# Kernel tuning notes

Hardware: AMD Instinct MI355X
Metric: run time of the kernel (lower is better)

The kernel has to match this reference:

```python
import jax, jax.numpy as jnp
import numpy as np

N_NODES = 50000
N_EDGES = 1600000
IN_DIM, HID_DIM, OUT_DIM = 512, 128, 16


def spmm(edge_src, edge_dst, edge_vals, x):
    # sparse.mm(A, x): out[dst] += A[dst, src] * x[src]
    msgs = edge_vals[:, None] * x[edge_src]  # [E, D]
    return jax.ops.segment_sum(msgs, edge_dst, num_segments=N_NODES)


def setup_inputs() -> dict:
    key = jax.random.key(0)
    k1, k2, k3, k4, k5, k6 = jax.random.split(key, 6)
    feature = jax.random.normal(k1, (N_NODES, IN_DIM), dtype=jnp.float32)
    edge_src = jax.random.randint(k2, (N_EDGES,), 0, N_NODES, dtype=jnp.int32)
    edge_dst = jax.random.randint(k3, (N_EDGES,), 0, N_NODES, dtype=jnp.int32)
    edge_vals = jax.random.uniform(k4, (N_EDGES,), dtype=jnp.float32)
    # kaiming_uniform-style init: bound = sqrt(6 / fan_in) (a=sqrt(5) omitted for simplicity of scale)
    b1 = float(np.sqrt(6.0 / IN_DIM))
    b2 = float(np.sqrt(6.0 / HID_DIM))
    W1 = jax.random.uniform(k5, (IN_DIM, HID_DIM), dtype=jnp.float32, minval=-b1, maxval=b1)
    W2 = jax.random.uniform(k6, (HID_DIM, OUT_DIM), dtype=jnp.float32, minval=-b2, maxval=b2)
    return {"feature": feature, "edge_src": edge_src, "edge_dst": edge_dst,
            "edge_vals": edge_vals, "W1": W1, "W2": W2}


def reference(feature, edge_src, edge_dst, edge_vals, W1, W2):
    # layer 1: dense matmul -> sparse aggregation -> ReLU
    h = jax.nn.relu(spmm(edge_src, edge_dst, edge_vals, feature @ W1))
    # layer 2
    out = spmm(edge_src, edge_dst, edge_vals, h @ W2)
    return out
```

## Files before the change

kernel.cpp:

```cpp
#include <hip/hip_runtime.h>

#define N_NODES 50000
#define N_EDGES 1600000
#define IN_DIM 512
#define HID_DIM 128
#define OUT_DIM 16

#define BKT_SHIFT 6
#define BKT_NODES 64
#define NB ((N_NODES + BKT_NODES - 1) / BKT_NODES)
#define SC_EDGES 8192
#define SC_BLOCKS ((N_EDGES + SC_EDGES - 1) / SC_EDGES)
#define PREP_BLOCKS ((IN_DIM * HID_DIM + 1023) / 1024)
#define NS_CAP 2560
#define MG_GEMM_BLOCKS ((N_NODES + 127) / 128)

typedef __attribute__((ext_vector_type(8))) __bf16 bf16x8;
typedef __attribute__((ext_vector_type(4))) __bf16 bf16x4;
typedef __attribute__((ext_vector_type(8))) unsigned short ushort8;
typedef __attribute__((ext_vector_type(4))) float f32x4;
typedef __attribute__((ext_vector_type(2))) float f32x2;

static __device__ __forceinline__ unsigned short f2bf(float x) {
    unsigned int u = __float_as_uint(x);
    u += 0x7FFFu + ((u >> 16) & 1u);
    return (unsigned short)(u >> 16);
}
static __device__ __forceinline__ float bf2f(unsigned short v) {
    return __uint_as_float(((unsigned int)v) << 16);
}
static __device__ __forceinline__ unsigned char f2fp8(float x) {
    int pk = __builtin_amdgcn_cvt_pk_fp8_f32(x, x, 0, false);
    return (unsigned char)(pk & 0xFF);
}

__device__ inline int wave_incl_scan(int v) {
    #pragma unroll
    for (int off = 1; off < 64; off <<= 1) {
        int x = __shfl_up(v, off, 64);
        if ((threadIdx.x & 63) >= off) v += x;
    }
    return v;
}


__global__ void zero_bcnt_kernel(int* __restrict__ bcnt) {
    int t = threadIdx.x;
    if (t < NB) bcnt[t] = 0;
}

__global__ __launch_bounds__(1024) void hist_prep_kernel(const int* __restrict__ dst,
                                                         int* __restrict__ bcnt,
                                                         int* __restrict__ blk_hist_T,
                                                         const float* __restrict__ W1,
                                                         unsigned short* __restrict__ Wt) {
    if (blockIdx.x >= SC_BLOCKS) {
        int i = (blockIdx.x - SC_BLOCKS) * 1024 + threadIdx.x;
        if (i < IN_DIM * HID_DIM) {
            int k = i >> 7, col = i & 127;
            Wt[(size_t)col * IN_DIM + k] = f2bf(W1[i]);
        }
        return;
    }
    __shared__ int lc[NB];
    const int t = threadIdx.x;
    for (int b = t; b < NB; b += 1024) lc[b] = 0;
    __syncthreads();
    const int eb = blockIdx.x * SC_EDGES + t * 8;
    #pragma unroll
    for (int q = 0; q < 2; q++) {
        int e0 = eb + q * 4;
        if (e0 + 4 <= N_EDGES) {
            int4 d4 = *(const int4*)&dst[e0];
            atomicAdd(&lc[d4.x >> BKT_SHIFT], 1);
            atomicAdd(&lc[d4.y >> BKT_SHIFT], 1);
            atomicAdd(&lc[d4.z >> BKT_SHIFT], 1);
            atomicAdd(&lc[d4.w >> BKT_SHIFT], 1);
        } else {
            for (int k = 0; k < 4; k++) {
                int e = e0 + k;
                if (e < N_EDGES) atomicAdd(&lc[dst[e] >> BKT_SHIFT], 1);
            }
        }
    }
    __syncthreads();
    for (int b = t; b < NB; b += 1024) {
        int c = lc[b];
        blk_hist_T[(size_t)b * SC_BLOCKS + blockIdx.x] = c;
        if (c) atomicAdd(&bcnt[b], c);
    }
}

__global__ __launch_bounds__(1024) void bucket_scan_kernel(const int* __restrict__ bcnt,
                                                           int* __restrict__ bucket_ptr) {
    __shared__ int wsums[16];
    const int t = threadIdx.x;
    const int lane = t & 63, wid = t >> 6;
    int v = (t < NB) ? bcnt[t] : 0;
    int incl = wave_incl_scan(v);
    if (lane == 63) wsums[wid] = incl;
    __syncthreads();
    if (wid == 0) {
        int wv = (lane < 16) ? wsums[lane] : 0;
        int ws = wave_incl_scan(wv);
        if (lane < 16) wsums[lane] = ws;
    }
    __syncthreads();
    int woff = wid ? wsums[wid - 1] : 0;
    int excl = woff + incl - v;
    if (t < NB) bucket_ptr[t] = excl;
    if (t == NB - 1) bucket_ptr[NB] = excl + v;
}

__global__ __launch_bounds__(512) void base_scan_kernel(const int* __restrict__ bucket_ptr,
                                                        int* __restrict__ blk_hist_T) {
    const int lane = threadIdx.x & 63;
    const int b = blockIdx.x * 8 + (threadIdx.x >> 6);
    if (b >= NB) return;
    int* row = blk_hist_T + (size_t)b * SC_BLOCKS;
    int carry = bucket_ptr[b];
    for (int c0 = 0; c0 < SC_BLOCKS; c0 += 64) {
        int idx = c0 + lane;
        int v = (idx < SC_BLOCKS) ? row[idx] : 0;
        int incl = wave_incl_scan(v);
        if (idx < SC_BLOCKS) row[idx] = carry + incl - v;
        carry += __shfl(incl, 63, 64);
    }
}


#define G1_XSTR 72
#define G1_BSTR 72
__global__ __launch_bounds__(512) void scatter_gemm1_kernel(const float* __restrict__ X,
                                                            const unsigned short* __restrict__ Wt,
                                                            unsigned char* __restrict__ h0,
                                                            const int* __restrict__ src,
                                                            const int* __restrict__ dst,
                                                            const float* __restrict__ val,
                                                            const int* __restrict__ blk_hist_T,
                                                            int2* __restrict__ pairs_bkt) {
    if (blockIdx.x < MG_GEMM_BLOCKS) {
        __shared__ __align__(16) unsigned short Xs[128 * G1_XSTR];
        __shared__ __align__(16) unsigned short Bs[128 * G1_BSTR];
        const int t = threadIdx.x;
        const int lane = t & 63;
        const int wave = t >> 6;
        const int wr = wave >> 2;
        const int wc = wave & 3;
        const int c = lane & 15, g = lane >> 4;
        const int m0 = blockIdx.x * 128;

        f32x4 acc[4][2];
        #pragma unroll
        for (int mt = 0; mt < 4; mt++)
            #pragma unroll
            for (int nt = 0; nt < 2; nt++) acc[mt][nt] = (f32x4){0.f, 0.f, 0.f, 0.f};

        float4 xrA[4], xrB[4];
        ushort8 brA[2], brB[2];

        #define G1_LOAD(XR, BR, kt)                                                          \
            _Pragma("unroll")                                                                \
            for (int p = 0; p < 4; p++) {                                                    \
                int idx = p * 512 + t;                                                       \
                int xrow = idx >> 4, xseg = idx & 15;                                        \
                int grow = m0 + xrow; grow = (grow < N_NODES) ? grow : (N_NODES - 1);        \
                XR[p] = *(const float4*)&X[(size_t)grow * IN_DIM + (kt) * 64 + xseg * 4];    \
            }                                                                                \
            _Pragma("unroll")                                                                \
            for (int p = 0; p < 2; p++) {                                                    \
                int idx = p * 512 + t;                                                       \
                int bcol = idx >> 3, bseg = idx & 7;                                         \
                BR[p] = *(const ushort8*)&Wt[(size_t)bcol * IN_DIM + (kt) * 64 + bseg * 8];  \
            }

        #define G1_WRITE(XR, BR)                                                             \
            _Pragma("unroll")                                                                \
            for (int p = 0; p < 4; p++) {                                                    \
                int idx = p * 512 + t;                                                       \
                int xrow = idx >> 4, xseg = idx & 15;                                        \
                bf16x4 xw;                                                                   \
                xw[0] = (__bf16)XR[p].x; xw[1] = (__bf16)XR[p].y;                            \
                xw[2] = (__bf16)XR[p].z; xw[3] = (__bf16)XR[p].w;                            \
                *(bf16x4*)&Xs[xrow * G1_XSTR + xseg * 4] = xw;                               \
            }                                                                                \
            _Pragma("unroll")                                                                \
            for (int p = 0; p < 2; p++) {                                                    \
                int idx = p * 512 + t;                                                       \
                int bcol = idx >> 3, bseg = idx & 7;                                         \
                *(ushort8*)&Bs[bcol * G1_BSTR + bseg * 8] = BR[p];                           \
            }

        G1_LOAD(xrA, brA, 0)
        G1_LOAD(xrB, brB, 1)
        #pragma unroll
        for (int kt = 0; kt < 8; kt++) {
            if (kt & 1) { G1_WRITE(xrB, brB) } else { G1_WRITE(xrA, brA) }
            __syncthreads();
            if (kt + 2 < 8) {
                if (kt & 1) { G1_LOAD(xrB, brB, kt + 2) } else { G1_LOAD(xrA, brA, kt + 2) }
            }
            #pragma unroll
            for (int ks = 0; ks < 2; ks++) {
                bf16x8 bf[2];
                #pragma unroll
                for (int nt = 0; nt < 2; nt++) {
                    int col = wc * 32 + nt * 16 + c;
                    bf[nt] = *(const bf16x8*)&Bs[col * G1_BSTR + ks * 32 + g * 8];
                }
                #pragma unroll
                for (int mt = 0; mt < 4; mt++) {
                    bf16x8 af = *(const bf16x8*)&Xs[(wr * 64 + mt * 16 + c) * G1_XSTR + ks * 32 + g * 8];
                    #pragma unroll
                    for (int nt = 0; nt < 2; nt++)
                        acc[mt][nt] = __builtin_amdgcn_mfma_f32_16x16x32_bf16(af, bf[nt],
                                                                              acc[mt][nt], 0, 0, 0);
                }
            }
            __syncthreads();
        }
        #undef G1_LOAD
        #undef G1_WRITE

        #pragma unroll
        for (int mt = 0; mt < 4; mt++) {
            #pragma unroll
            for (int r = 0; r < 4; r++) {
                int row = m0 + wr * 64 + mt * 16 + g * 4 + r;
                if (row < N_NODES) {
                    #pragma unroll
                    for (int nt = 0; nt < 2; nt++) {
                        int col = wc * 32 + nt * 16 + c;
                        h0[(size_t)row * HID_DIM + col] = f2fp8(acc[mt][nt][r]);
                    }
                }
            }
        }
    } else {
        __shared__ int cbase[NB];
        const int sb = blockIdx.x - MG_GEMM_BLOCKS;
        const int t = threadIdx.x;
        for (int b = t; b < NB; b += 512)
            cbase[b] = blk_hist_T[(size_t)b * SC_BLOCKS + sb];
        __syncthreads();
        const int eb = sb * SC_EDGES + t * 16;
        #pragma unroll
        for (int q = 0; q < 4; q++) {
            int e0 = eb + q * 4;
            if (e0 + 4 <= N_EDGES) {
                int4 s4 = *(const int4*)&src[e0];
                int4 d4 = *(const int4*)&dst[e0];
                float4 v4 = *(const float4*)&val[e0];
                #pragma unroll
                for (int k = 0; k < 4; k++) {
                    int ss = (k == 0) ? s4.x : (k == 1) ? s4.y : (k == 2) ? s4.z : s4.w;
                    int dd = (k == 0) ? d4.x : (k == 1) ? d4.y : (k == 2) ? d4.z : d4.w;
                    float vv = (k == 0) ? v4.x : (k == 1) ? v4.y : (k == 2) ? v4.z : v4.w;
                    int b = dd >> BKT_SHIFT, dl = dd & (BKT_NODES - 1);
                    int pos = atomicAdd(&cbase[b], 1);
                    int2 pr;
                    pr.x = ss | (dl << 16);
                    pr.y = __float_as_int(vv);
                    pairs_bkt[pos] = pr;
                }
            } else {
                for (int k = 0; k < 4; k++) {
                    int e = e0 + k;
                    if (e < N_EDGES) {
                        int dd = dst[e];
                        int b = dd >> BKT_SHIFT, dl = dd & (BKT_NODES - 1);
                        int pos = atomicAdd(&cbase[b], 1);
                        int2 pr;
                        pr.x = src[e] | (dl << 16);
                        pr.y = __float_as_int(val[e]);
                        pairs_bkt[pos] = pr;
                    }
                }
            }
        }
    }
}

__global__ __launch_bounds__(512) void node_sort_fused_kernel(const int2* __restrict__ pairs_bkt,
                                                              const int* __restrict__ bucket_ptr,
                                                              int* __restrict__ row_ptr,
                                                              int2* __restrict__ pairs) {
    __shared__ int cnt[BKT_NODES];
    __shared__ int base[BKT_NODES];
    __shared__ int2 stage[NS_CAP];
    const int t = threadIdx.x;
    const int b = blockIdx.x;
    const int s = bucket_ptr[b], e = bucket_ptr[b + 1];
    if (t < BKT_NODES) cnt[t] = 0;
    __syncthreads();
    for (int i = s + t; i < e; i += 512)
        atomicAdd(&cnt[pairs_bkt[i].x >> 16], 1);
    __syncthreads();
    if (t < BKT_NODES) {
        int v = cnt[t];
        int incl = wave_incl_scan(v);
        base[t] = s + incl - v;
    }
    __syncthreads();
    if (t < BKT_NODES) {
        int n = b * BKT_NODES + t;
        if (n < N_NODES) row_ptr[n] = base[t];
        cnt[t] = 0;
    }
    if (b == NB - 1 && t == 0) row_ptr[N_NODES] = N_EDGES;
    __syncthreads();
    for (int i = s + t; i < e; i += 512) {
        int2 pr = pairs_bkt[i];
        int dl = pr.x >> 16;
        int p = base[dl] + atomicAdd(&cnt[dl], 1);
        int loc = p - s;
        if (loc < NS_CAP) stage[loc] = pr;
        else pairs[p] = pr;
    }
    __syncthreads();
    const int lim = min(e - s, NS_CAP);
    for (int j = t; j < lim; j += 512)
        pairs[s + j] = stage[j];
}


__global__ __launch_bounds__(256) void spmm1_node_kernel(const unsigned char* __restrict__ h0,
                                                         const int* __restrict__ row_ptr,
                                                         const int2* __restrict__ pairs,
                                                         unsigned short* __restrict__ h) {
    const int wid = __builtin_amdgcn_readfirstlane(threadIdx.x >> 6);
    const int n = blockIdx.x * 4 + wid;
    const int lane = threadIdx.x & 63;
    const int s = row_ptr[n], e = row_ptr[n + 1];
    const unsigned char* h0l = h0 + lane * 2;
    float ax = 0.f, ay = 0.f;
    for (int base = s; base < e; base += 8) {
        float vv[8];
        const unsigned char* rp[8];
        #pragma unroll
        for (int k = 0; k < 8; k++) {
            int idx = base + k;
            int cidx = (idx < e) ? idx : (e - 1);
            int2 pr = pairs[cidx];
            vv[k] = (idx < e) ? __int_as_float(pr.y) : 0.f;
            rp[k] = h0l + (size_t)(pr.x & 0xFFFF) * HID_DIM;
        }
        unsigned short gg[8];
        #pragma unroll
        for (int k = 0; k < 8; k++) gg[k] = *(const unsigned short*)rp[k];
        #pragma unroll
        for (int k = 0; k < 8; k++) {
            f32x2 f = __builtin_amdgcn_cvt_pk_f32_fp8((int)gg[k], false);
            ax += vv[k] * f.x;
            ay += vv[k] * f.y;
        }
    }
    unsigned int w = ((unsigned int)f2bf(fmaxf(ay, 0.f)) << 16) | f2bf(fmaxf(ax, 0.f));
    ((unsigned int*)(h + (size_t)n * HID_DIM))[lane] = w;
}

__global__ __launch_bounds__(256) void gemm2_kernel(const unsigned short* __restrict__ H,
                                                    const float* __restrict__ W2,
                                                    unsigned short* __restrict__ C) {
    __shared__ float Hs[16][132];
    __shared__ float Ws[128][16];
    const int t = threadIdx.x;
    const int n0 = blockIdx.x * 16;
    #pragma unroll
    for (int p = 0; p < 2; p++) {
        int idx = p * 256 + t;
        ((float4*)Ws)[idx] = ((const float4*)W2)[idx];
    }
    {
        int row = t >> 4, seg = t & 15;
        int gr = n0 + row;
        ushort8 hv = {0, 0, 0, 0, 0, 0, 0, 0};
        if (gr < N_NODES) hv = *(const ushort8*)&H[(size_t)gr * HID_DIM + seg * 8];
        #pragma unroll
        for (int j = 0; j < 8; j++) Hs[row][seg * 8 + j] = bf2f(hv[j]);
    }
    __syncthreads();
    const int nl = t >> 4, j = t & 15;
    float acc = 0.f;
    #pragma unroll 8
    for (int k = 0; k < 128; k++) acc += Hs[nl][k] * Ws[k][j];
    int n = n0 + nl;
    if (n < N_NODES) C[(size_t)n * OUT_DIM + j] = f2bf(acc);
}

__global__ __launch_bounds__(256) void spmm2_node_kernel(const unsigned short* __restrict__ h2,
                                                         const int* __restrict__ row_ptr,
                                                         const int2* __restrict__ pairs,
                                                         float* __restrict__ out) {
    const int idx = blockIdx.x * 256 + threadIdx.x;
    const int n = idx >> 4;
    const int d = idx & 15;
    if (n >= N_NODES) return;
    const int s = row_ptr[n], e = row_ptr[n + 1];
    float acc = 0.f;
    int i = s;
    for (; i + 4 <= e; i += 4) {
        int2 p0 = pairs[i], p1 = pairs[i + 1], p2 = pairs[i + 2], p3 = pairs[i + 3];
        unsigned short g0 = h2[(size_t)(p0.x & 0xFFFF) * OUT_DIM + d];
        unsigned short g1 = h2[(size_t)(p1.x & 0xFFFF) * OUT_DIM + d];
        unsigned short g2 = h2[(size_t)(p2.x & 0xFFFF) * OUT_DIM + d];
        unsigned short g3 = h2[(size_t)(p3.x & 0xFFFF) * OUT_DIM + d];
        acc += __int_as_float(p0.y) * bf2f(g0) + __int_as_float(p1.y) * bf2f(g1)
             + __int_as_float(p2.y) * bf2f(g2) + __int_as_float(p3.y) * bf2f(g3);
    }
    for (; i < e; i++) {
        int2 pr = pairs[i];
        acc += __int_as_float(pr.y) * bf2f(h2[(size_t)(pr.x & 0xFFFF) * OUT_DIM + d]);
    }
    out[(size_t)n * OUT_DIM + d] = acc;
}


extern "C" void kernel_launch(void* const* d_in, const int* in_sizes, int n_in,
                              void* d_out, int out_size, void* d_ws, size_t ws_size,
                              hipStream_t stream) {
    const float* feature   = (const float*)d_in[0];
    const int*   edge_src  = (const int*)d_in[1];
    const int*   edge_dst  = (const int*)d_in[2];
    const float* edge_vals = (const float*)d_in[3];
    const float* W1        = (const float*)d_in[4];
    const float* W2        = (const float*)d_in[5];
    float* out = (float*)d_out;

    char* ws = (char*)d_ws;
    size_t off = 0;
    auto alloc = [&](size_t bytes) {
        void* p = ws + off;
        off += (bytes + 255) & ~(size_t)255;
        return p;
    };
    unsigned char*  h0    = (unsigned char*)alloc((size_t)N_NODES * HID_DIM);
    unsigned short* Wt    = (unsigned short*)alloc((size_t)IN_DIM * HID_DIM * 2);
    unsigned short* h     = (unsigned short*)alloc((size_t)N_NODES * HID_DIM * 2);
    unsigned short* h2    = (unsigned short*)alloc((size_t)N_NODES * OUT_DIM * 2);
    int*   bcnt           = (int*)alloc((size_t)NB * 4);
    int*   bucket_ptr     = (int*)alloc((size_t)(NB + 1) * 4);
    int*   blk_hist_T     = (int*)alloc((size_t)NB * SC_BLOCKS * 4);
    int*   row_ptr        = (int*)alloc((size_t)(N_NODES + 1) * 4);
    int2*  pairs_bkt      = (int2*)alloc((size_t)N_EDGES * 8);
    int2*  pairs          = (int2*)alloc((size_t)N_EDGES * 8);

    zero_bcnt_kernel<<<1, 1024, 0, stream>>>(bcnt);
    hist_prep_kernel<<<SC_BLOCKS + PREP_BLOCKS, 1024, 0, stream>>>(edge_dst, bcnt, blk_hist_T,
                                                                   W1, Wt);
    bucket_scan_kernel<<<1, 1024, 0, stream>>>(bcnt, bucket_ptr);
    base_scan_kernel<<<(NB + 7) / 8, 512, 0, stream>>>(bucket_ptr, blk_hist_T);
    scatter_gemm1_kernel<<<MG_GEMM_BLOCKS + SC_BLOCKS, 512, 0, stream>>>(
        feature, Wt, h0, edge_src, edge_dst, edge_vals, blk_hist_T, pairs_bkt);
    node_sort_fused_kernel<<<NB, 512, 0, stream>>>(pairs_bkt, bucket_ptr, row_ptr, pairs);

    spmm1_node_kernel<<<(N_NODES + 3) / 4, 256, 0, stream>>>(h0, row_ptr, pairs, h);
    gemm2_kernel<<<(N_NODES + 15) / 16, 256, 0, stream>>>(h, W2, h2);
    spmm2_node_kernel<<<(N_NODES * 16 + 255) / 256, 256, 0, stream>>>(h2, row_ptr, pairs, out);
}
```

Measured before the change: 140.2 us.

## Fold bucket scan into base scan and split scatter from GEMM1 kernel

Removes the single-block bucket_scan kernel: each base_scan block now computes the prefix of bucket counts it needs redundantly, in one wave, and writes bucket_ptr itself. The fused scatter+GEMM1 kernel is split into a dedicated 1024-thread bucket scatter kernel and a standalone GEMM1 kernel. The aim is to cut one launch and serial dependency, and to give each kernel its own resource footprint. In exchange, the two workloads no longer overlap inside one launch, and there is redundant scan work across blocks.

```diff
diff --git a/kernel.cpp b/kernel.cpp
--- a/kernel.cpp
+++ b/kernel.cpp
@@ -13,7 +13,6 @@
 #define SC_BLOCKS ((N_EDGES + SC_EDGES - 1) / SC_EDGES)
 #define PREP_BLOCKS ((IN_DIM * HID_DIM + 1023) / 1024)
 #define NS_CAP 2560
-#define MG_GEMM_BLOCKS ((N_NODES + 127) / 128)
 
 typedef __attribute__((ext_vector_type(8))) __bf16 bf16x8;
 typedef __attribute__((ext_vector_type(4))) __bf16 bf16x4;
@@ -91,34 +90,34 @@
     }
 }
 
-__global__ __launch_bounds__(1024) void bucket_scan_kernel(const int* __restrict__ bcnt,
-                                                           int* __restrict__ bucket_ptr) {
-    __shared__ int wsums[16];
-    const int t = threadIdx.x;
-    const int lane = t & 63, wid = t >> 6;
-    int v = (t < NB) ? bcnt[t] : 0;
-    int incl = wave_incl_scan(v);
-    if (lane == 63) wsums[wid] = incl;
-    __syncthreads();
-    if (wid == 0) {
-        int wv = (lane < 16) ? wsums[lane] : 0;
-        int ws = wave_incl_scan(wv);
-        if (lane < 16) wsums[lane] = ws;
-    }
-    __syncthreads();
-    int woff = wid ? wsums[wid - 1] : 0;
-    int excl = woff + incl - v;
-    if (t < NB) bucket_ptr[t] = excl;
-    if (t == NB - 1) bucket_ptr[NB] = excl + v;
-}
-
-__global__ __launch_bounds__(512) void base_scan_kernel(const int* __restrict__ bucket_ptr,
+__global__ __launch_bounds__(512) void base_scan_kernel(const int* __restrict__ bcnt,
+                                                        int* __restrict__ bucket_ptr,
                                                         int* __restrict__ blk_hist_T) {
-    const int lane = threadIdx.x & 63;
-    const int b = blockIdx.x * 8 + (threadIdx.x >> 6);
+    __shared__ int sbase[8];
+    const int t = threadIdx.x;
+    const int lane = t & 63, wv = t >> 6;
+    const int b0 = blockIdx.x * 8;
+    if (wv == 0) {
+        int carry = 0;
+        const int lim = b0 + 8;
+        for (int c0 = 0; c0 < lim; c0 += 64) {
+            int idx = c0 + lane;
+            int v = (idx < lim && idx < NB) ? bcnt[idx] : 0;
+            int incl = wave_incl_scan(v);
+            int excl = carry + incl - v;
+            if (idx >= b0 && idx < lim && idx < NB) {
+                sbase[idx - b0] = excl;
+                bucket_ptr[idx] = excl;
+                if (idx == NB - 1) bucket_ptr[NB] = excl + v;
+            }
+            carry += __shfl(incl, 63, 64);
+        }
+    }
+    __syncthreads();
+    const int b = b0 + wv;
     if (b >= NB) return;
     int* row = blk_hist_T + (size_t)b * SC_BLOCKS;
-    int carry = bucket_ptr[b];
+    int carry = sbase[wv];
     for (int c0 = 0; c0 < SC_BLOCKS; c0 += 64) {
         int idx = c0 + lane;
         int v = (idx < SC_BLOCKS) ? row[idx] : 0;
@@ -128,153 +127,150 @@
     }
 }
 
+__global__ __launch_bounds__(1024) void bucket_scatter_kernel(const int* __restrict__ src,
+                                                              const int* __restrict__ dst,
+                                                              const float* __restrict__ val,
+                                                              const int* __restrict__ blk_hist_T,
+                                                              int2* __restrict__ pairs_bkt) {
+    __shared__ int cbase[NB];
+    const int t = threadIdx.x;
+    for (int b = t; b < NB; b += 1024)
+        cbase[b] = blk_hist_T[(size_t)b * SC_BLOCKS + blockIdx.x];
+    __syncthreads();
+    const int eb = blockIdx.x * SC_EDGES + t * 8;
+    #pragma unroll
+    for (int q = 0; q < 2; q++) {
+        int e0 = eb + q * 4;
+        if (e0 + 4 <= N_EDGES) {
+            int4 s4 = *(const int4*)&src[e0];
+            int4 d4 = *(const int4*)&dst[e0];
+            float4 v4 = *(const float4*)&val[e0];
+            #pragma unroll
+            for (int k = 0; k < 4; k++) {
+                int ss = (k == 0) ? s4.x : (k == 1) ? s4.y : (k == 2) ? s4.z : s4.w;
+                int dd = (k == 0) ? d4.x : (k == 1) ? d4.y : (k == 2) ? d4.z : d4.w;
+                float vv = (k == 0) ? v4.x : (k == 1) ? v4.y : (k == 2) ? v4.z : v4.w;
+                int b = dd >> BKT_SHIFT, dl = dd & (BKT_NODES - 1);
+                int pos = atomicAdd(&cbase[b], 1);
+                int2 pr;
+                pr.x = ss | (dl << 16);
+                pr.y = __float_as_int(vv);
+                pairs_bkt[pos] = pr;
+            }
+        } else {
+            for (int k = 0; k < 4; k++) {
+                int e = e0 + k;
+                if (e < N_EDGES) {
+                    int dd = dst[e];
+                    int b = dd >> BKT_SHIFT, dl = dd & (BKT_NODES - 1);
+                    int pos = atomicAdd(&cbase[b], 1);
+                    int2 pr;
+                    pr.x = src[e] | (dl << 16);
+                    pr.y = __float_as_int(val[e]);
+                    pairs_bkt[pos] = pr;
+                }
+            }
+        }
+    }
+}
 
 #define G1_XSTR 72
 #define G1_BSTR 72
-__global__ __launch_bounds__(512) void scatter_gemm1_kernel(const float* __restrict__ X,
-                                                            const unsigned short* __restrict__ Wt,
-                                                            unsigned char* __restrict__ h0,
-                                                            const int* __restrict__ src,
-                                                            const int* __restrict__ dst,
-                                                            const float* __restrict__ val,
-                                                            const int* __restrict__ blk_hist_T,
-                                                            int2* __restrict__ pairs_bkt) {
-    if (blockIdx.x < MG_GEMM_BLOCKS) {
-        __shared__ __align__(16) unsigned short Xs[128 * G1_XSTR];
-        __shared__ __align__(16) unsigned short Bs[128 * G1_BSTR];
-        const int t = threadIdx.x;
-        const int lane = t & 63;
-        const int wave = t >> 6;
-        const int wr = wave >> 2;
-        const int wc = wave & 3;
-        const int c = lane & 15, g = lane >> 4;
-        const int m0 = blockIdx.x * 128;
-
-        f32x4 acc[4][2];
-        #pragma unroll
-        for (int mt = 0; mt < 4; mt++)
+__global__ __launch_bounds__(512) void gemm1_kernel(const float* __restrict__ X,
+                                                    const unsigned short* __restrict__ Wt,
+                                                    unsigned char* __restrict__ h0) {
+    __shared__ __align__(16) unsigned short Xs[128 * G1_XSTR];
+    __shared__ __align__(16) unsigned short Bs[128 * G1_BSTR];
+    const int t = threadIdx.x;
+    const int lane = t & 63;
+    const int wave = t >> 6;
+    const int wr = wave >> 2;
+    const int wc = wave & 3;
+    const int c = lane & 15, g = lane >> 4;
+    const int m0 = blockIdx.x * 128;
+
+    f32x4 acc[4][2];
+    #pragma unroll
+    for (int mt = 0; mt < 4; mt++)
+        #pragma unroll
+        for (int nt = 0; nt < 2; nt++) acc[mt][nt] = (f32x4){0.f, 0.f, 0.f, 0.f};
+
+    float4 xrA[4], xrB[4];
+    ushort8 brA[2], brB[2];
+
+    #define G1_LOAD(XR, BR, kt)                                                          \
+        _Pragma("unroll")                                                                \
+        for (int p = 0; p < 4; p++) {                                                    \
+            int idx = p * 512 + t;                                                       \
+            int xrow = idx >> 4, xseg = idx & 15;                                        \
+            int grow = m0 + xrow; grow = (grow < N_NODES) ? grow : (N_NODES - 1);        \
+            XR[p] = *(const float4*)&X[(size_t)grow * IN_DIM + (kt) * 64 + xseg * 4];    \
+        }                                                                                \
+        _Pragma("unroll")                                                                \
+        for (int p = 0; p < 2; p++) {                                                    \
+            int idx = p * 512 + t;                                                       \
+            int bcol = idx >> 3, bseg = idx & 7;                                         \
+            BR[p] = *(const ushort8*)&Wt[(size_t)bcol * IN_DIM + (kt) * 64 + bseg * 8];  \
+        }
+
+    #define G1_WRITE(XR, BR)                                                             \
+        _Pragma("unroll")                                                                \
+        for (int p = 0; p < 4; p++) {                                                    \
+            int idx = p * 512 + t;                                                       \
+            int xrow = idx >> 4, xseg = idx & 15;                                        \
+            bf16x4 xw;                                                                   \
+            xw[0] = (__bf16)XR[p].x; xw[1] = (__bf16)XR[p].y;                            \
+            xw[2] = (__bf16)XR[p].z; xw[3] = (__bf16)XR[p].w;                            \
+            *(bf16x4*)&Xs[xrow * G1_XSTR + xseg * 4] = xw;                               \
+        }                                                                                \
+        _Pragma("unroll")                                                                \
+        for (int p = 0; p < 2; p++) {                                                    \
+            int idx = p * 512 + t;                                                       \
+            int bcol = idx >> 3, bseg = idx & 7;                                         \
+            *(ushort8*)&Bs[bcol * G1_BSTR + bseg * 8] = BR[p];                           \
+        }
+
+    G1_LOAD(xrA, brA, 0)
+    G1_LOAD(xrB, brB, 1)
+    #pragma unroll
+    for (int kt = 0; kt < 8; kt++) {
+        if (kt & 1) { G1_WRITE(xrB, brB) } else { G1_WRITE(xrA, brA) }
+        __syncthreads();
+        if (kt + 2 < 8) {
+            if (kt & 1) { G1_LOAD(xrB, brB, kt + 2) } else { G1_LOAD(xrA, brA, kt + 2) }
+        }
+        #pragma unroll
+        for (int ks = 0; ks < 2; ks++) {
+            bf16x8 bf[2];
             #pragma unroll
-            for (int nt = 0; nt < 2; nt++) acc[mt][nt] = (f32x4){0.f, 0.f, 0.f, 0.f};
-
-        float4 xrA[4], xrB[4];
-        ushort8 brA[2], brB[2];
-
-        #define G1_LOAD(XR, BR, kt)                                                          \
-            _Pragma("unroll")                                                                \
-            for (int p = 0; p < 4; p++) {                                                    \
-                int idx = p * 512 + t;                                                       \
-                int xrow = idx >> 4, xseg = idx & 15;                                        \
-                int grow = m0 + xrow; grow = (grow < N_NODES) ? grow : (N_NODES - 1);        \
-                XR[p] = *(const float4*)&X[(size_t)grow * IN_DIM + (kt) * 64 + xseg * 4];    \
-            }                                                                                \
-            _Pragma("unroll")                                                                \
-            for (int p = 0; p < 2; p++) {                                                    \
-                int idx = p * 512 + t;                                                       \
-                int bcol = idx >> 3, bseg = idx & 7;                                         \
-                BR[p] = *(const ushort8*)&Wt[(size_t)bcol * IN_DIM + (kt) * 64 + bseg * 8];  \
-            }
-
-        #define G1_WRITE(XR, BR)                                                             \
-            _Pragma("unroll")                                                                \
-            for (int p = 0; p < 4; p++) {                                                    \
-                int idx = p * 512 + t;                                                       \
-                int xrow = idx >> 4, xseg = idx & 15;                                        \
-                bf16x4 xw;                                                                   \
-                xw[0] = (__bf16)XR[p].x; xw[1] = (__bf16)XR[p].y;                            \
-                xw[2] = (__bf16)XR[p].z; xw[3] = (__bf16)XR[p].w;                            \
-                *(bf16x4*)&Xs[xrow * G1_XSTR + xseg * 4] = xw;                               \
-            }                                                                                \
-            _Pragma("unroll")                                                                \
-            for (int p = 0; p < 2; p++) {                                                    \
-                int idx = p * 512 + t;                                                       \
-                int bcol = idx >> 3, bseg = idx & 7;                                         \
-                *(ushort8*)&Bs[bcol * G1_BSTR + bseg * 8] = BR[p];                           \
-            }
-
-        G1_LOAD(xrA, brA, 0)
-        G1_LOAD(xrB, brB, 1)
-        #pragma unroll
-        for (int kt = 0; kt < 8; kt++) {
-            if (kt & 1) { G1_WRITE(xrB, brB) } else { G1_WRITE(xrA, brA) }
-            __syncthreads();
-            if (kt + 2 < 8) {
-                if (kt & 1) { G1_LOAD(xrB, brB, kt + 2) } else { G1_LOAD(xrA, brA, kt + 2) }
+            for (int nt = 0; nt < 2; nt++) {
+                int col = wc * 32 + nt * 16 + c;
+                bf[nt] = *(const bf16x8*)&Bs[col * G1_BSTR + ks * 32 + g * 8];
             }
             #pragma unroll
-            for (int ks = 0; ks < 2; ks++) {
-                bf16x8 bf[2];
+            for (int mt = 0; mt < 4; mt++) {
+                bf16x8 af = *(const bf16x8*)&Xs[(wr * 64 + mt * 16 + c) * G1_XSTR + ks * 32 + g * 8];
+                #pragma unroll
+                for (int nt = 0; nt < 2; nt++)
+                    acc[mt][nt] = __builtin_amdgcn_mfma_f32_16x16x32_bf16(af, bf[nt],
+                                                                          acc[mt][nt], 0, 0, 0);
+            }
+        }
+        __syncthreads();
+    }
+    #undef G1_LOAD
+    #undef G1_WRITE
+
+    #pragma unroll
+    for (int mt = 0; mt < 4; mt++) {
+        #pragma unroll
+        for (int r = 0; r < 4; r++) {
+            int row = m0 + wr * 64 + mt * 16 + g * 4 + r;
+            if (row < N_NODES) {
                 #pragma unroll
                 for (int nt = 0; nt < 2; nt++) {
                     int col = wc * 32 + nt * 16 + c;
-                    bf[nt] = *(const bf16x8*)&Bs[col * G1_BSTR + ks * 32 + g * 8];
-                }
-                #pragma unroll
-                for (int mt = 0; mt < 4; mt++) {
-                    bf16x8 af = *(const bf16x8*)&Xs[(wr * 64 + mt * 16 + c) * G1_XSTR + ks * 32 + g * 8];
-                    #pragma unroll
-                    for (int nt = 0; nt < 2; nt++)
-                        acc[mt][nt] = __builtin_amdgcn_mfma_f32_16x16x32_bf16(af, bf[nt],
-                                                                              acc[mt][nt], 0, 0, 0);
-                }
-            }
-            __syncthreads();
-        }
-        #undef G1_LOAD
-        #undef G1_WRITE
-
-        #pragma unroll
-        for (int mt = 0; mt < 4; mt++) {
-            #pragma unroll
-            for (int r = 0; r < 4; r++) {
-                int row = m0 + wr * 64 + mt * 16 + g * 4 + r;
-                if (row < N_NODES) {
-                    #pragma unroll
-                    for (int nt = 0; nt < 2; nt++) {
-                        int col = wc * 32 + nt * 16 + c;
-                        h0[(size_t)row * HID_DIM + col] = f2fp8(acc[mt][nt][r]);
-                    }
-                }
-            }
-        }
-    } else {
-        __shared__ int cbase[NB];
-        const int sb = blockIdx.x - MG_GEMM_BLOCKS;
-        const int t = threadIdx.x;
-        for (int b = t; b < NB; b += 512)
-            cbase[b] = blk_hist_T[(size_t)b * SC_BLOCKS + sb];
-        __syncthreads();
-        const int eb = sb * SC_EDGES + t * 16;
-        #pragma unroll
-        for (int q = 0; q < 4; q++) {
-            int e0 = eb + q * 4;
-            if (e0 + 4 <= N_EDGES) {
-                int4 s4 = *(const int4*)&src[e0];
-                int4 d4 = *(const int4*)&dst[e0];
-                float4 v4 = *(const float4*)&val[e0];
-                #pragma unroll
-                for (int k = 0; k < 4; k++) {
-                    int ss = (k == 0) ? s4.x : (k == 1) ? s4.y : (k == 2) ? s4.z : s4.w;
-                    int dd = (k == 0) ? d4.x : (k == 1) ? d4.y : (k == 2) ? d4.z : d4.w;
-                    float vv = (k == 0) ? v4.x : (k == 1) ? v4.y : (k == 2) ? v4.z : v4.w;
-                    int b = dd >> BKT_SHIFT, dl = dd & (BKT_NODES - 1);
-                    int pos = atomicAdd(&cbase[b], 1);
-                    int2 pr;
-                    pr.x = ss | (dl << 16);
-                    pr.y = __float_as_int(vv);
-                    pairs_bkt[pos] = pr;
-                }
-            } else {
-                for (int k = 0; k < 4; k++) {
-                    int e = e0 + k;
-                    if (e < N_EDGES) {
-                        int dd = dst[e];
-                        int b = dd >> BKT_SHIFT, dl = dd & (BKT_NODES - 1);
-                        int pos = atomicAdd(&cbase[b], 1);
-                        int2 pr;
-                        pr.x = src[e] | (dl << 16);
-                        pr.y = __float_as_int(val[e]);
-                        pairs_bkt[pos] = pr;
-                    }
+                    h0[(size_t)row * HID_DIM + col] = f2fp8(acc[mt][nt][r]);
                 }
             }
         }
@@ -448,10 +444,10 @@
     zero_bcnt_kernel<<<1, 1024, 0, stream>>>(bcnt);
     hist_prep_kernel<<<SC_BLOCKS + PREP_BLOCKS, 1024, 0, stream>>>(edge_dst, bcnt, blk_hist_T,
                                                                    W1, Wt);
-    bucket_scan_kernel<<<1, 1024, 0, stream>>>(bcnt, bucket_ptr);
-    base_scan_kernel<<<(NB + 7) / 8, 512, 0, stream>>>(bucket_ptr, blk_hist_T);
-    scatter_gemm1_kernel<<<MG_GEMM_BLOCKS + SC_BLOCKS, 512, 0, stream>>>(
-        feature, Wt, h0, edge_src, edge_dst, edge_vals, blk_hist_T, pairs_bkt);
+    base_scan_kernel<<<(NB + 7) / 8, 512, 0, stream>>>(bcnt, bucket_ptr, blk_hist_T);
+    bucket_scatter_kernel<<<SC_BLOCKS, 1024, 0, stream>>>(edge_src, edge_dst, edge_vals,
+                                                          blk_hist_T, pairs_bkt);
+    gemm1_kernel<<<(N_NODES + 127) / 128, 512, 0, stream>>>(feature, Wt, h0);
     node_sort_fused_kernel<<<NB, 512, 0, stream>>>(pairs_bkt, bucket_ptr, row_ptr, pairs);
 
     spmm1_node_kernel<<<(N_NODES + 3) / 4, 256, 0, stream>>>(h0, row_ptr, pairs, h);
```

New measurement: 144.6 us. 3.2% more time.
